# Performance work log

Hardware: AMD Instinct MI355X
Metric: run time of the kernel (lower is better)

## Reference

```python
import jax, jax.numpy as jnp
import numpy as np
from math import factorial

# ---- static config: mirrors FullTensorProductSparse("64x0e + 64x1o", "32x0e + 32x1o", leading_shape=(2048,)) ----
IRREPS1 = [(64, 0, 1), (64, 1, -1)]   # (mul, l, parity); already regrouped
IRREPS2 = [(32, 0, 1), (32, 1, -1)]
N_LEAD = 2048


def _su2_cg_coeff(j1, m1, j2, m2, j3, m3):
    # Racah formula, identical to e3nn._su2_clebsch_gordan_coeff
    if m3 != m1 + m2:
        return 0.0
    f = factorial
    vmin = max(-j1 + j2 + m3, -j1 + m1, 0)
    vmax = min(j2 + j3 + m1, j3 - j1 + j2, j3 + m3)
    C = ((2.0 * j3 + 1.0) * f(j3 + j1 - j2) * f(j3 - j1 + j2) * f(j1 + j2 - j3)
         * f(j3 + m3) * f(j3 - m3)
         / (f(j1 + j2 + j3 + 1) * f(j1 - m1) * f(j1 + m1) * f(j2 - m2) * f(j2 + m2))) ** 0.5
    S = 0.0
    for v in range(vmin, vmax + 1):
        S += (-1.0) ** (v + j2 + m2) * f(j2 + j3 + m1 - v) * f(j1 - m1 + v) / (
            f(v) * f(j3 - j1 + j2 - v) * f(j3 + m3 - v) * f(v + j1 - j2 - m3))
    return C * S


def _su2_cg(j1, j2, j3):
    mat = np.zeros((2 * j1 + 1, 2 * j2 + 1, 2 * j3 + 1), dtype=np.float64)
    if abs(j1 - j2) <= j3 <= j1 + j2:
        for m1 in range(-j1, j1 + 1):
            for m2 in range(-j2, j2 + 1):
                if abs(m1 + m2) <= j3:
                    mat[j1 + m1, j2 + m2, j3 + m1 + m2] = _su2_cg_coeff(j1, m1, j2, m2, j3, m1 + m2)
    return mat / (2 * j3 + 1) ** 0.5


def _change_basis_real_to_complex(l):
    q = np.zeros((2 * l + 1, 2 * l + 1), dtype=np.complex128)
    for m in range(-l, 0):
        q[l + m, l + abs(m)] = 2 ** -0.5
        q[l + m, l - abs(m)] = -1j * 2 ** -0.5
    q[l, l] = 1.0
    for m in range(1, l + 1):
        q[l + m, l + abs(m)] = (-1) ** m * 2 ** -0.5
        q[l + m, l - abs(m)] = 1j * (-1) ** m * 2 ** -0.5
    return (-1j) ** l * q  # phase makes the real-basis CG coefficients real


def wigner_3j(l1, l2, l3):
    # real-basis Wigner 3j, identical to e3nn.o3.wigner_3j
    Q1 = _change_basis_real_to_complex(l1)
    Q2 = _change_basis_real_to_complex(l2)
    Q3 = _change_basis_real_to_complex(l3)
    C = _su2_cg(l1, l2, l3).astype(np.complex128)
    C = np.einsum('ij,kl,mn,ikn->jlm', Q1, Q2, np.conj(Q3.T), C)
    assert np.abs(C.imag).max() < 1e-8
    C = C.real
    return C / np.linalg.norm(C)


def _paths():
    # mirrors the (l1,l2,l3) path construction in __init__ (no filter_ir_out)
    paths = []
    off1 = 0
    for mul1, l1, p1 in IRREPS1:
        d1 = 2 * l1 + 1
        off2 = 0
        for mul2, l2, p2 in IRREPS2:
            d2 = 2 * l2 + 1
            for l3 in range(abs(l1 - l2), l1 + l2 + 1):
                p3 = p1 * p2
                cg = wigner_3j(l1, l2, l3) * np.sqrt(2 * l3 + 1)  # 'component' normalization
                paths.append((off1, mul1, d1, off2, mul2, d2, l3, p3, cg))
            off2 += mul2 * d2
        off1 += mul1 * d1
    return paths


def setup_inputs() -> dict:
    key = jax.random.key(0)
    k1, k2 = jax.random.split(key)
    d_in1 = sum(m * (2 * l + 1) for m, l, _ in IRREPS1)
    d_in2 = sum(m * (2 * l + 1) for m, l, _ in IRREPS2)
    return {
        'input1': jax.random.normal(k1, (N_LEAD, d_in1), dtype=jnp.float32),
        'input2': jax.random.normal(k2, (N_LEAD, d_in2), dtype=jnp.float32),
    }


def reference(input1, input2):
    n = input1.shape[0]
    chunks, keys = [], []
    for off1, mul1, d1, off2, mul2, d2, l3, p3, cg in _paths():
        d3 = 2 * l3 + 1
        # faithful to the torch module: raw row-major reshape of the (n, mul*dim)
        # irrep slice into (dim, mul, n) (no transpose), exactly as in forward().
        x1 = input1[:, off1:off1 + mul1 * d1].reshape(d1, mul1, n)
        x2 = input2[:, off2:off2 + mul2 * d2].reshape(d2, mul2, n)
        C = jnp.asarray(cg, dtype=input1.dtype)
        # dense CG contraction == the sparse (m1,m2,m3) loop: CG is zero off-pattern
        chunk = jnp.einsum('ijk,iun,jvn->kuvn', C, x1, x2)  # [d3, mul1, mul2, n]
        chunk = jnp.moveaxis(chunk, 0, -1).reshape(n, mul1 * mul2 * d3)
        chunks.append(chunk)
        keys.append((l3, -p3 * (-1) ** l3))  # Irrep canonical sort key: 0e,0o,1o,1e,2e,2o
    inv = sorted(range(len(keys)), key=lambda i: keys[i])  # stable argsort == Irreps.sort().inv
    return jnp.concatenate([chunks[i] for i in inv], axis=-1)
```

## Files before the change

kernel.cpp:

```cpp
#include <hip/hip_runtime.h>
#include <complex>
#include <cmath>


static double fct(int n) { double r = 1.0; for (int i = 2; i <= n; ++i) r *= i; return r; }

static double su2_cg_coeff(int j1, int m1, int j2, int m2, int j3, int m3) {
    if (m3 != m1 + m2) return 0.0;
    int vmin = std::max(std::max(-j1 + j2 + m3, -j1 + m1), 0);
    int vmax = std::min(std::min(j2 + j3 + m1, j3 - j1 + j2), j3 + m3);
    double C = std::sqrt((2.0 * j3 + 1.0) * fct(j3 + j1 - j2) * fct(j3 - j1 + j2) * fct(j1 + j2 - j3)
                         * fct(j3 + m3) * fct(j3 - m3)
                         / (fct(j1 + j2 + j3 + 1) * fct(j1 - m1) * fct(j1 + m1) * fct(j2 - m2) * fct(j2 + m2)));
    double S = 0.0;
    for (int v = vmin; v <= vmax; ++v) {
        double sgn = ((v + j2 + m2) & 1) ? -1.0 : 1.0;
        S += sgn * fct(j2 + j3 + m1 - v) * fct(j1 - m1 + v)
             / (fct(v) * fct(j3 - j1 + j2 - v) * fct(j3 + m3 - v) * fct(v + j1 - j2 - m3));
    }
    return C * S;
}

static void cob(int l, std::complex<double> q[5][5]) {
    for (int a = 0; a < 5; ++a) for (int b = 0; b < 5; ++b) q[a][b] = 0.0;
    const double is2 = 1.0 / std::sqrt(2.0);
    for (int m = -l; m < 0; ++m) {
        q[l + m][l - m] = is2;
        q[l + m][l + m] = std::complex<double>(0.0, -is2);
    }
    q[l][l] = 1.0;
    for (int m = 1; m <= l; ++m) {
        double sgn = (m & 1) ? -1.0 : 1.0;
        q[l + m][l + m] = sgn * is2;
        q[l + m][l - m] = std::complex<double>(0.0, sgn * is2);
    }
    std::complex<double> ph;
    switch (l & 3) {
        case 0: ph = 1.0; break;
        case 1: ph = std::complex<double>(0.0, -1.0); break;
        case 2: ph = -1.0; break;
        default: ph = std::complex<double>(0.0, 1.0); break;
    }
    for (int a = 0; a < 5; ++a) for (int b = 0; b < 5; ++b) q[a][b] *= ph;
}

static void wigner3j(int l1, int l2, int l3, double* out) {
    int d1 = 2 * l1 + 1, d2 = 2 * l2 + 1, d3 = 2 * l3 + 1;
    double csu2[5][5][5] = {};
    for (int m1 = -l1; m1 <= l1; ++m1)
        for (int m2 = -l2; m2 <= l2; ++m2)
            if (std::abs(m1 + m2) <= l3)
                csu2[l1 + m1][l2 + m2][l3 + m1 + m2] =
                    su2_cg_coeff(l1, m1, l2, m2, l3, m1 + m2) / std::sqrt(2.0 * l3 + 1.0);
    std::complex<double> Q1[5][5], Q2[5][5], Q3[5][5];
    cob(l1, Q1); cob(l2, Q2); cob(l3, Q3);
    double nrm = 0.0;
    for (int j = 0; j < d1; ++j)
        for (int l = 0; l < d2; ++l)
            for (int m = 0; m < d3; ++m) {
                std::complex<double> s = 0.0;
                for (int i = 0; i < d1; ++i)
                    for (int k = 0; k < d2; ++k)
                        for (int n = 0; n < d3; ++n)
                            s += Q1[i][j] * Q2[k][l] * std::conj(Q3[n][m]) * csu2[i][k][n];
                out[(j * d2 + l) * d3 + m] = s.real();
                nrm += s.real() * s.real();
            }
    nrm = std::sqrt(nrm);
    for (int t = 0; t < d1 * d2 * d3; ++t) out[t] /= nrm;
}

struct CGTab {
    float cA;
    float B[9];
    float Cjk[9];
    float Dik[9];
    float E[27];
    float F[45];
};


__global__ __launch_bounds__(256) void ftp_kernel(const float* __restrict__ in1,
                                                  const float* __restrict__ in2,
                                                  float* __restrict__ out,
                                                  CGTab cg) {
    const int t = threadIdx.x;
    const int r = blockIdx.x;
    const int u = r >> 5;
    const int v = r & 31;
    float* __restrict__ orow = out + (size_t)r * 32768;

#pragma unroll
    for (int h = 0; h < 2; ++h) {
        const int nn = h * 1024 + t * 4;

        alignas(16) float a0q[4], b0q[4], a1q[3][4], b1q[3][4];
        *(float4*)a0q = *(const float4*)&in1[(u * 32 + (nn >> 6)) * 256 + (nn & 63)];
        *(float4*)b0q = *(const float4*)&in2[(v * 64 + (nn >> 5)) * 128 + (nn & 31)];
#pragma unroll
        for (int i = 0; i < 3; ++i) {
            const int f   = i * 131072 + u * 2048 + nn;
            const int row = f / 192, col = f - row * 192;
            *(float4*)a1q[i] = *(const float4*)&in1[row * 256 + 64 + col];
        }
#pragma unroll
        for (int j = 0; j < 3; ++j) {
            const int g   = j * 65536 + v * 2048 + nn;
            const int row = g / 96, col = g - row * 96;
            *(float4*)b1q[j] = *(const float4*)&in2[row * 128 + 32 + col];
        }

        alignas(16) float o[20];

#pragma unroll
        for (int d = 0; d < 4; ++d) o[d] = cg.cA * a0q[d] * b0q[d];
        *(float4*)&orow[nn] = *(const float4*)o;

#pragma unroll
        for (int d = 0; d < 4; ++d) {
            float s = 0.f;
#pragma unroll
            for (int i = 0; i < 3; ++i)
#pragma unroll
                for (int j = 0; j < 3; ++j)
                    s = fmaf(cg.B[i * 3 + j], a1q[i][d] * b1q[j][d], s);
            o[d] = s;
        }
        *(float4*)&orow[2048 + nn] = *(const float4*)o;

#pragma unroll
        for (int d = 0; d < 4; ++d)
#pragma unroll
            for (int k = 0; k < 3; ++k) {
                float s = 0.f;
#pragma unroll
                for (int j = 0; j < 3; ++j) s = fmaf(cg.Cjk[j * 3 + k], b1q[j][d], s);
                o[d * 3 + k] = a0q[d] * s;
            }
#pragma unroll
        for (int s4 = 0; s4 < 3; ++s4)
            *(float4*)&orow[4096 + 3 * nn + 4 * s4] = *(const float4*)&o[4 * s4];

#pragma unroll
        for (int d = 0; d < 4; ++d)
#pragma unroll
            for (int k = 0; k < 3; ++k) {
                float s = 0.f;
#pragma unroll
                for (int i = 0; i < 3; ++i) s = fmaf(cg.Dik[i * 3 + k], a1q[i][d], s);
                o[d * 3 + k] = b0q[d] * s;
            }
#pragma unroll
        for (int s4 = 0; s4 < 3; ++s4)
            *(float4*)&orow[10240 + 3 * nn + 4 * s4] = *(const float4*)&o[4 * s4];

#pragma unroll
        for (int d = 0; d < 4; ++d)
#pragma unroll
            for (int k = 0; k < 3; ++k) {
                float s = 0.f;
#pragma unroll
                for (int i = 0; i < 3; ++i)
#pragma unroll
                    for (int j = 0; j < 3; ++j)
                        s = fmaf(cg.E[(i * 3 + j) * 3 + k], a1q[i][d] * b1q[j][d], s);
                o[d * 3 + k] = s;
            }
#pragma unroll
        for (int s4 = 0; s4 < 3; ++s4)
            *(float4*)&orow[16384 + 3 * nn + 4 * s4] = *(const float4*)&o[4 * s4];

#pragma unroll
        for (int d = 0; d < 4; ++d)
#pragma unroll
            for (int k = 0; k < 5; ++k) {
                float s = 0.f;
#pragma unroll
                for (int i = 0; i < 3; ++i)
#pragma unroll
                    for (int j = 0; j < 3; ++j)
                        s = fmaf(cg.F[(i * 3 + j) * 5 + k], a1q[i][d] * b1q[j][d], s);
                o[d * 5 + k] = s;
            }
#pragma unroll
        for (int s4 = 0; s4 < 5; ++s4)
            *(float4*)&orow[22528 + 5 * nn + 4 * s4] = *(const float4*)&o[4 * s4];
    }
}


extern "C" void kernel_launch(void* const* d_in, const int* in_sizes, int n_in,
                              void* d_out, int out_size, void* d_ws, size_t ws_size,
                              hipStream_t stream) {
    const float* in1 = (const float*)d_in[0];
    const float* in2 = (const float*)d_in[1];
    float* out = (float*)d_out;

    CGTab cg;
    double w[45];
    const double s3 = std::sqrt(3.0), s5 = std::sqrt(5.0);

    wigner3j(0, 0, 0, w);
    cg.cA = (float)(w[0] * 1.0);

    wigner3j(1, 1, 0, w);
    for (int i = 0; i < 3; ++i)
        for (int j = 0; j < 3; ++j) cg.B[i * 3 + j] = (float)(w[(i * 3 + j)] * 1.0);

    wigner3j(0, 1, 1, w);
    for (int j = 0; j < 3; ++j)
        for (int k = 0; k < 3; ++k) cg.Cjk[j * 3 + k] = (float)(w[j * 3 + k] * s3);

    wigner3j(1, 0, 1, w);
    for (int i = 0; i < 3; ++i)
        for (int k = 0; k < 3; ++k) cg.Dik[i * 3 + k] = (float)(w[i * 3 + k] * s3);

    wigner3j(1, 1, 1, w);
    for (int t = 0; t < 27; ++t) cg.E[t] = (float)(w[t] * s3);

    wigner3j(1, 1, 2, w);
    for (int t = 0; t < 45; ++t) cg.F[t] = (float)(w[t] * s5);

    dim3 grid(2048, 1, 1);
    dim3 block(256, 1, 1);
    ftp_kernel<<<grid, block, 0, stream>>>(in1, in2, out, cg);
}
```

Baseline: 299.8 us.

## Assign one output float4 per thread so every store is fully coalesced

Each thread now produces one contiguous float4 of output instead of each block looping over a whole output row. Interleaved multi-component sections (3- and 5-wide) are computed per thread from scalar loads of one or two neighbouring n positions, and the needed components are selected. This makes the write stream fully coalesced and launches far more threads to saturate memory bandwidth. In exchange there are redundant input loads and recomputation, since neighbouring threads reload overlapping inputs, and branch divergence at section boundaries.

Result: slower. 314.5 us (+4.9%).

```diff
diff --git a/kernel.cpp b/kernel.cpp
--- a/kernel.cpp
+++ b/kernel.cpp
@@ -80,112 +80,186 @@
 };
 
 
+__device__ __forceinline__ float lda0(const float* __restrict__ in1, int u, int nn) {
+    return in1[u * 8192 + ((nn >> 6) << 8) + (nn & 63)];
+}
+__device__ __forceinline__ float ldb0(const float* __restrict__ in2, int v, int nn) {
+    return in2[v * 8192 + ((nn >> 5) << 7) + (nn & 31)];
+}
+__device__ __forceinline__ float lda1(const float* __restrict__ in1, int u, int i, int nn) {
+    const int f = i * 131072 + u * 2048 + nn;
+    const int row = f / 192;
+    return in1[row * 256 + 64 + (f - row * 192)];
+}
+__device__ __forceinline__ float ldb1(const float* __restrict__ in2, int v, int j, int nn) {
+    const int g = j * 65536 + v * 2048 + nn;
+    const int row = g / 96;
+    return in2[row * 128 + 32 + (g - row * 96)];
+}
+
 __global__ __launch_bounds__(256) void ftp_kernel(const float* __restrict__ in1,
                                                   const float* __restrict__ in2,
                                                   float* __restrict__ out,
                                                   CGTab cg) {
-    const int t = threadIdx.x;
-    const int r = blockIdx.x;
-    const int u = r >> 5;
-    const int v = r & 31;
-    float* __restrict__ orow = out + (size_t)r * 32768;
-
-#pragma unroll
-    for (int h = 0; h < 2; ++h) {
-        const int nn = h * 1024 + t * 4;
-
-        alignas(16) float a0q[4], b0q[4], a1q[3][4], b1q[3][4];
-        *(float4*)a0q = *(const float4*)&in1[(u * 32 + (nn >> 6)) * 256 + (nn & 63)];
-        *(float4*)b0q = *(const float4*)&in2[(v * 64 + (nn >> 5)) * 128 + (nn & 31)];
+    const int idx  = blockIdx.x * 256 + threadIdx.x;
+    const int r    = idx >> 13;
+    const int col4 = idx & 8191;
+    const int u    = r >> 5;
+    const int v    = r & 31;
+    float4* __restrict__ orow4 = (float4*)(out + (size_t)r * 32768);
+
+    alignas(16) float o[4];
+
+    if (col4 < 512) {
+        const int nn = col4 << 2;
+        alignas(16) float a0q[4], b0q[4];
+        *(float4*)a0q = *(const float4*)&in1[u * 8192 + ((nn >> 6) << 8) + (nn & 63)];
+        *(float4*)b0q = *(const float4*)&in2[v * 8192 + ((nn >> 5) << 7) + (nn & 31)];
+#pragma unroll
+        for (int e = 0; e < 4; ++e) o[e] = cg.cA * a0q[e] * b0q[e];
+    } else if (col4 < 1024) {
+        const int nn = (col4 - 512) << 2;
+        alignas(16) float a1q[3][4], b1q[3][4];
 #pragma unroll
         for (int i = 0; i < 3; ++i) {
-            const int f   = i * 131072 + u * 2048 + nn;
-            const int row = f / 192, col = f - row * 192;
-            *(float4*)a1q[i] = *(const float4*)&in1[row * 256 + 64 + col];
+            const int f = i * 131072 + u * 2048 + nn, row = f / 192;
+            *(float4*)a1q[i] = *(const float4*)&in1[row * 256 + 64 + (f - row * 192)];
         }
 #pragma unroll
         for (int j = 0; j < 3; ++j) {
-            const int g   = j * 65536 + v * 2048 + nn;
-            const int row = g / 96, col = g - row * 96;
-            *(float4*)b1q[j] = *(const float4*)&in2[row * 128 + 32 + col];
-        }
-
-        alignas(16) float o[20];
-
-#pragma unroll
-        for (int d = 0; d < 4; ++d) o[d] = cg.cA * a0q[d] * b0q[d];
-        *(float4*)&orow[nn] = *(const float4*)o;
-
-#pragma unroll
-        for (int d = 0; d < 4; ++d) {
+            const int g = j * 65536 + v * 2048 + nn, row = g / 96;
+            *(float4*)b1q[j] = *(const float4*)&in2[row * 128 + 32 + (g - row * 96)];
+        }
+#pragma unroll
+        for (int e = 0; e < 4; ++e) {
             float s = 0.f;
 #pragma unroll
             for (int i = 0; i < 3; ++i)
 #pragma unroll
                 for (int j = 0; j < 3; ++j)
-                    s = fmaf(cg.B[i * 3 + j], a1q[i][d] * b1q[j][d], s);
-            o[d] = s;
-        }
-        *(float4*)&orow[2048 + nn] = *(const float4*)o;
-
-#pragma unroll
-        for (int d = 0; d < 4; ++d)
+                    s = fmaf(cg.B[i * 3 + j], a1q[i][e] * b1q[j][e], s);
+            o[e] = s;
+        }
+    } else if (col4 < 2560) {
+        const int c0 = (col4 - 1024) << 2;
+        const int n0 = c0 / 3, k0 = c0 - n0 * 3;
+        const int n1 = (n0 < 2047) ? n0 + 1 : 2047;
+        const float a0s0 = lda0(in1, u, n0), a0s1 = lda0(in1, u, n1);
+        float b1s[3][2];
+#pragma unroll
+        for (int j = 0; j < 3; ++j) { b1s[j][0] = ldb1(in2, v, j, n0); b1s[j][1] = ldb1(in2, v, j, n1); }
+        float s[2][3];
+#pragma unroll
+        for (int sel = 0; sel < 2; ++sel)
 #pragma unroll
             for (int k = 0; k < 3; ++k) {
-                float s = 0.f;
-#pragma unroll
-                for (int j = 0; j < 3; ++j) s = fmaf(cg.Cjk[j * 3 + k], b1q[j][d], s);
-                o[d * 3 + k] = a0q[d] * s;
+                float acc = 0.f;
+#pragma unroll
+                for (int j = 0; j < 3; ++j) acc = fmaf(cg.Cjk[j * 3 + k], b1s[j][sel], acc);
+                s[sel][k] = (sel ? a0s1 : a0s0) * acc;
             }
 #pragma unroll
-        for (int s4 = 0; s4 < 3; ++s4)
-            *(float4*)&orow[4096 + 3 * nn + 4 * s4] = *(const float4*)&o[4 * s4];
-
-#pragma unroll
-        for (int d = 0; d < 4; ++d)
+        for (int e = 0; e < 4; ++e) {
+            const float r0 = s[(e + 0) / 3][(e + 0) % 3];
+            const float r1 = s[(e + 1) / 3][(e + 1) % 3];
+            const float r2 = s[(e + 2) / 3][(e + 2) % 3];
+            o[e] = (k0 == 0) ? r0 : ((k0 == 1) ? r1 : r2);
+        }
+    } else if (col4 < 4096) {
+        const int c0 = (col4 - 2560) << 2;
+        const int n0 = c0 / 3, k0 = c0 - n0 * 3;
+        const int n1 = (n0 < 2047) ? n0 + 1 : 2047;
+        const float b0s0 = ldb0(in2, v, n0), b0s1 = ldb0(in2, v, n1);
+        float a1s[3][2];
+#pragma unroll
+        for (int i = 0; i < 3; ++i) { a1s[i][0] = lda1(in1, u, i, n0); a1s[i][1] = lda1(in1, u, i, n1); }
+        float s[2][3];
+#pragma unroll
+        for (int sel = 0; sel < 2; ++sel)
 #pragma unroll
             for (int k = 0; k < 3; ++k) {
-                float s = 0.f;
-#pragma unroll
-                for (int i = 0; i < 3; ++i) s = fmaf(cg.Dik[i * 3 + k], a1q[i][d], s);
-                o[d * 3 + k] = b0q[d] * s;
+                float acc = 0.f;
+#pragma unroll
+                for (int i = 0; i < 3; ++i) acc = fmaf(cg.Dik[i * 3 + k], a1s[i][sel], acc);
+                s[sel][k] = (sel ? b0s1 : b0s0) * acc;
             }
 #pragma unroll
-        for (int s4 = 0; s4 < 3; ++s4)
-            *(float4*)&orow[10240 + 3 * nn + 4 * s4] = *(const float4*)&o[4 * s4];
-
-#pragma unroll
-        for (int d = 0; d < 4; ++d)
-#pragma unroll
-            for (int k = 0; k < 3; ++k) {
-                float s = 0.f;
-#pragma unroll
-                for (int i = 0; i < 3; ++i)
-#pragma unroll
-                    for (int j = 0; j < 3; ++j)
-                        s = fmaf(cg.E[(i * 3 + j) * 3 + k], a1q[i][d] * b1q[j][d], s);
-                o[d * 3 + k] = s;
-            }
-#pragma unroll
-        for (int s4 = 0; s4 < 3; ++s4)
-            *(float4*)&orow[16384 + 3 * nn + 4 * s4] = *(const float4*)&o[4 * s4];
-
-#pragma unroll
-        for (int d = 0; d < 4; ++d)
-#pragma unroll
-            for (int k = 0; k < 5; ++k) {
-                float s = 0.f;
-#pragma unroll
-                for (int i = 0; i < 3; ++i)
-#pragma unroll
-                    for (int j = 0; j < 3; ++j)
-                        s = fmaf(cg.F[(i * 3 + j) * 5 + k], a1q[i][d] * b1q[j][d], s);
-                o[d * 5 + k] = s;
-            }
-#pragma unroll
-        for (int s4 = 0; s4 < 5; ++s4)
-            *(float4*)&orow[22528 + 5 * nn + 4 * s4] = *(const float4*)&o[4 * s4];
-    }
+        for (int e = 0; e < 4; ++e) {
+            const float r0 = s[(e + 0) / 3][(e + 0) % 3];
+            const float r1 = s[(e + 1) / 3][(e + 1) % 3];
+            const float r2 = s[(e + 2) / 3][(e + 2) % 3];
+            o[e] = (k0 == 0) ? r0 : ((k0 == 1) ? r1 : r2);
+        }
+    } else if (col4 < 5632) {
+        const int c0 = (col4 - 4096) << 2;
+        const int n0 = c0 / 3, k0 = c0 - n0 * 3;
+        const int n1 = (n0 < 2047) ? n0 + 1 : 2047;
+        float a1s[3][2], b1s[3][2];
+#pragma unroll
+        for (int i = 0; i < 3; ++i) { a1s[i][0] = lda1(in1, u, i, n0); a1s[i][1] = lda1(in1, u, i, n1); }
+#pragma unroll
+        for (int j = 0; j < 3; ++j) { b1s[j][0] = ldb1(in2, v, j, n0); b1s[j][1] = ldb1(in2, v, j, n1); }
+        float s[2][3];
+#pragma unroll
+        for (int sel = 0; sel < 2; ++sel) {
+#pragma unroll
+            for (int k = 0; k < 3; ++k) s[sel][k] = 0.f;
+#pragma unroll
+            for (int i = 0; i < 3; ++i)
+#pragma unroll
+                for (int j = 0; j < 3; ++j) {
+                    const float p = a1s[i][sel] * b1s[j][sel];
+#pragma unroll
+                    for (int k = 0; k < 3; ++k)
+                        s[sel][k] = fmaf(cg.E[(i * 3 + j) * 3 + k], p, s[sel][k]);
+                }
+        }
+#pragma unroll
+        for (int e = 0; e < 4; ++e) {
+            const float r0 = s[(e + 0) / 3][(e + 0) % 3];
+            const float r1 = s[(e + 1) / 3][(e + 1) % 3];
+            const float r2 = s[(e + 2) / 3][(e + 2) % 3];
+            o[e] = (k0 == 0) ? r0 : ((k0 == 1) ? r1 : r2);
+        }
+    } else {
+        const int c0 = (col4 - 5632) << 2;
+        const int n0 = c0 / 5, k0 = c0 - n0 * 5;
+        const int n1 = (n0 < 2047) ? n0 + 1 : 2047;
+        float a1s[3][2], b1s[3][2];
+#pragma unroll
+        for (int i = 0; i < 3; ++i) { a1s[i][0] = lda1(in1, u, i, n0); a1s[i][1] = lda1(in1, u, i, n1); }
+#pragma unroll
+        for (int j = 0; j < 3; ++j) { b1s[j][0] = ldb1(in2, v, j, n0); b1s[j][1] = ldb1(in2, v, j, n1); }
+        float s[2][5];
+#pragma unroll
+        for (int sel = 0; sel < 2; ++sel) {
+#pragma unroll
+            for (int k = 0; k < 5; ++k) s[sel][k] = 0.f;
+#pragma unroll
+            for (int i = 0; i < 3; ++i)
+#pragma unroll
+                for (int j = 0; j < 3; ++j) {
+                    const float p = a1s[i][sel] * b1s[j][sel];
+#pragma unroll
+                    for (int k = 0; k < 5; ++k)
+                        s[sel][k] = fmaf(cg.F[(i * 3 + j) * 5 + k], p, s[sel][k]);
+                }
+        }
+#pragma unroll
+        for (int e = 0; e < 4; ++e) {
+            const float r0 = s[(e + 0) / 5][(e + 0) % 5];
+            const float r1 = s[(e + 1) / 5][(e + 1) % 5];
+            const float r2 = s[(e + 2) / 5][(e + 2) % 5];
+            const float r3 = s[(e + 3) / 5][(e + 3) % 5];
+            const float r4 = s[(e + 4) / 5][(e + 4) % 5];
+            o[e] = (k0 == 0) ? r0
+                 : (k0 == 1) ? r1
+                 : (k0 == 2) ? r2
+                 : (k0 == 3) ? r3 : r4;
+        }
+    }
+
+    orow4[col4] = *(const float4*)o;
 }
 
 
@@ -221,7 +295,7 @@
     wigner3j(1, 1, 2, w);
     for (int t = 0; t < 45; ++t) cg.F[t] = (float)(w[t] * s5);
 
-    dim3 grid(2048, 1, 1);
+    dim3 grid(65536, 1, 1);
     dim3 block(256, 1, 1);
     ftp_kernel<<<grid, block, 0, stream>>>(in1, in2, out, cg);
 }
```
